# Performance work log

Measured on AMD Instinct MI355X. Metric: run time of the kernel, lower is better.

Reference implementation:

```python
import jax, jax.numpy as jnp
import numpy as np

SCORE_WEIGHT = 0.5
MAX_ITER = 20
PROJ_ITER = 5
RELAX_LR = 0.1
EPS = 1e-8

P, D, T, O, H, W = 256, 256, 2, 24, 240, 432


def setup_inputs() -> dict:
    key = jax.random.key(0)
    k1, k2, k3, k4, k5 = jax.random.split(key, 5)
    proposed_feature = jax.random.normal(k1, (P, D), dtype=jnp.float32)
    proposed_mask = (jax.random.uniform(k2, (P, H, W)) > 0.7).astype(jnp.float32)
    template_feature = jax.random.normal(k3, (T, O, D), dtype=jnp.float32)
    mask_last_occurence = (jax.random.uniform(k4, (O, H, W)) > 0.7).astype(jnp.float32)
    proposal_score = jax.random.uniform(k5, (P,), dtype=jnp.float32)
    return {
        "proposed_feature": proposed_feature,
        "proposed_mask": proposed_mask,
        "template_feature": template_feature,
        "mask_last_occurence": mask_last_occurence,
        "proposal_score": proposal_score,
    }


def relax_matching(C, max_iter=MAX_ITER, proj_iter=PROJ_INNER if False else PROJ_ITER, lr=RELAX_LR):
    """Projected-gradient relaxation of the assignment LP.
    Gradient step on <C, X>, then proj_iter alternating projections onto
    {X >= 0, X <= 1, row sums == 1}. Returns mean of iterates (sum(X_list)/len)."""
    K, N = C.shape
    X0 = jnp.full((K, N), 1.0 / N, dtype=C.dtype)

    def project(X):
        def body(_, X):
            X = jnp.clip(X, 0.0, 1.0)
            X = X / (jnp.sum(X, axis=1, keepdims=True) + EPS)
            return X
        return jax.lax.fori_loop(0, proj_iter, body, X)

    def step(X, _):
        X = project(X - lr * C)
        return X, X

    _, Xs = jax.lax.scan(step, X0, None, length=max_iter)
    return jnp.mean(Xs, axis=0)  # [K, N]


def reference(proposed_feature, proposed_mask, template_feature,
              mask_last_occurence, proposal_score):
    n_prop = proposed_mask.shape[0]
    n_tplt = mask_last_occurence.shape[0]
    h, w = proposed_mask.shape[1], proposed_mask.shape[2]

    # --- feature cosine similarity, averaged over template frames ---
    kf = proposed_feature / (jnp.linalg.norm(proposed_feature, axis=1, keepdims=True) + EPS)
    qf = template_feature / (jnp.linalg.norm(template_feature, axis=2, keepdims=True) + EPS)
    feature_sim = jnp.einsum('tod,pd->op', qf, kf) / template_feature.shape[0]  # [O, P]

    # --- pairwise binary-mask IoU without materializing [O*P, HW] ---
    A = mask_last_occurence.reshape(n_tplt, -1)  # [O, HW] templates
    B = proposed_mask.reshape(n_prop, -1)        # [P, HW] proposals
    inter = A @ B.T                              # [O, P]
    union = A.sum(axis=1)[:, None] + B.sum(axis=1)[None, :] - inter
    iou = inter / (union + EPS)

    sim_matrix = feature_sim * (1.0 - SCORE_WEIGHT) + iou * SCORE_WEIGHT
    # P > O so no padding branch; cost is [O, P]
    cost_matrix = -sim_matrix

    Ridx = relax_matching(cost_matrix)           # averaged iterates, [O, P]
    # training branch (is_test == 0)
    logic_mask = (Ridx > 0.01).astype(Ridx.dtype)
    binX = Ridx * logic_mask

    full_outmask = (binX @ B).reshape(n_tplt, h, w)                 # [O, H, W]
    match_score = jnp.max(jnp.clip(Ridx, 0.0, 1.0) * -cost_matrix, axis=1)  # [O]
    det_score = jnp.sum(proposal_score[None, :] * binX, axis=1)     # [O]
    return (full_outmask, match_score, det_score)
```

## Files before the change

### kernel.cpp

```cpp
#include <hip/hip_runtime.h>

#define HW 103680
#define WORDS 1620
#define NGRP 405
#define NP 256
#define NO 24
#define ND 256
#define EPSF 1e-8f
#define OUTM (NO*HW)

typedef unsigned long long u64;

__device__ __forceinline__ float waveRedSum(float v) {
  v += __int_as_float(__builtin_amdgcn_update_dpp(0, __float_as_int(v), 0x111, 0xf, 0xf, false));
  v += __int_as_float(__builtin_amdgcn_update_dpp(0, __float_as_int(v), 0x112, 0xf, 0xf, false));
  v += __int_as_float(__builtin_amdgcn_update_dpp(0, __float_as_int(v), 0x114, 0xf, 0xf, false));
  v += __int_as_float(__builtin_amdgcn_update_dpp(0, __float_as_int(v), 0x118, 0xf, 0xf, false));
  v += __int_as_float(__builtin_amdgcn_update_dpp(0, __float_as_int(v), 0x142, 0xf, 0xf, false));
  v += __int_as_float(__builtin_amdgcn_update_dpp(0, __float_as_int(v), 0x143, 0xf, 0xf, false));
  return __int_as_float(__builtin_amdgcn_readlane(__float_as_int(v), 63));
}
__device__ __forceinline__ float waveRedMax(float v) {
  int vi = __float_as_int(v);
  v = fmaxf(v, __int_as_float(__builtin_amdgcn_update_dpp(vi, vi, 0x111, 0xf, 0xf, false))); vi = __float_as_int(v);
  v = fmaxf(v, __int_as_float(__builtin_amdgcn_update_dpp(vi, vi, 0x112, 0xf, 0xf, false))); vi = __float_as_int(v);
  v = fmaxf(v, __int_as_float(__builtin_amdgcn_update_dpp(vi, vi, 0x114, 0xf, 0xf, false))); vi = __float_as_int(v);
  v = fmaxf(v, __int_as_float(__builtin_amdgcn_update_dpp(vi, vi, 0x118, 0xf, 0xf, false))); vi = __float_as_int(v);
  v = fmaxf(v, __int_as_float(__builtin_amdgcn_update_dpp(vi, vi, 0x142, 0xf, 0xf, false))); vi = __float_as_int(v);
  v = fmaxf(v, __int_as_float(__builtin_amdgcn_update_dpp(vi, vi, 0x143, 0xf, 0xf, false)));
  return __int_as_float(__builtin_amdgcn_readlane(__float_as_int(v), 63));
}

__device__ __forceinline__ void pack_group(const float* __restrict__ rp,
                                           u64* __restrict__ bits,
                                           int g, int lane, float4 v) {
  u64 m0 = __ballot(v.x != 0.0f);
  u64 m1 = __ballot(v.y != 0.0f);
  u64 m2 = __ballot(v.z != 0.0f);
  u64 m3 = __ballot(v.w != 0.0f);
  if (lane == 0) {
    ulonglong2 s0; s0.x = m0; s0.y = m1;
    ulonglong2 s1; s1.x = m2; s1.y = m3;
    *(ulonglong2*)(bits + g * 4)     = s0;
    *(ulonglong2*)(bits + g * 4 + 2) = s1;
  }
}

__global__ __launch_bounds__(256) void pack_kernel(const float* __restrict__ pm,
                                                   const float* __restrict__ ml,
                                                   u64* __restrict__ bbits,
                                                   u64* __restrict__ abits) {
  int row = blockIdx.y;
  int wir = (blockIdx.x * 256 + threadIdx.x) >> 6;
  int lane = threadIdx.x & 63;
  const float* rp;
  u64* bits;
  if (row < NP) { rp = pm + (size_t)row * HW;        bits = bbits + (size_t)row * WORDS; }
  else          { rp = ml + (size_t)(row - NP) * HW; bits = abits + (size_t)(row - NP) * WORDS; }
  int g = wir;
  while (g + 28 < NGRP) {
    float4 v0 = *(const float4*)(rp + g * 256 + lane * 4);
    float4 v1 = *(const float4*)(rp + (g + 28) * 256 + lane * 4);
    pack_group(rp, bits, g, lane, v0);
    pack_group(rp, bits, g + 28, lane, v1);
    g += 56;
  }
  if (g < NGRP) {
    float4 v0 = *(const float4*)(rp + g * 256 + lane * 4);
    pack_group(rp, bits, g, lane, v0);
  }
}

__global__ __launch_bounds__(256) void interfeat_kernel(const u64* __restrict__ ab,
                                                        const u64* __restrict__ bb,
                                                        const float* __restrict__ pf,
                                                        const float* __restrict__ tf,
                                                        float* __restrict__ C) {
  int wid = (blockIdx.x * 256 + threadIdx.x) >> 6;
  int lane = threadIdx.x & 63;
  int o = wid >> 8, p = wid & 255;
  float4 f = *(const float4*)(pf + p * ND + lane * 4);
  float4 a = *(const float4*)(tf + o * ND + lane * 4);
  float4 b = *(const float4*)(tf + (NO + o) * ND + lane * 4);
  const u64* arl = ab + (size_t)o * WORDS + lane;
  const u64* brl = bb + (size_t)p * WORDS + lane;
  int cnt = 0, ucnt = 0;
#pragma unroll 5
  for (int k = 0; k < 25; ++k) {
    u64 av = arl[k * 64], bv = brl[k * 64];
    cnt  += (int)__popcll(av & bv);
    ucnt += (int)__popcll(av | bv);
  }
  if (lane < WORDS - 1600) {
    u64 av = arl[1600], bv = brl[1600];
    cnt  += (int)__popcll(av & bv);
    ucnt += (int)__popcll(av | bv);
  }
  float inter = waveRedSum((float)cnt);
  float uni   = waveRedSum((float)ucnt);
  float nf = waveRedSum(f.x*f.x + f.y*f.y + f.z*f.z + f.w*f.w);
  float na = waveRedSum(a.x*a.x + a.y*a.y + a.z*a.z + a.w*a.w);
  float nb = waveRedSum(b.x*b.x + b.y*b.y + b.z*b.z + b.w*b.w);
  float d0 = waveRedSum(a.x*f.x + a.y*f.y + a.z*f.z + a.w*f.w);
  float d1 = waveRedSum(b.x*f.x + b.y*f.y + b.z*f.z + b.w*f.w);
  if (lane == 0) {
    float invf = 1.0f / (sqrtf(nf) + EPSF);
    float inva = 1.0f / (sqrtf(na) + EPSF);
    float invb = 1.0f / (sqrtf(nb) + EPSF);
    float fs  = (d0 * inva + d1 * invb) * invf * 0.5f;
    float iou = inter / (uni + EPSF);
    C[wid] = -(fs * 0.5f + iou * 0.5f);
  }
}

__global__ __launch_bounds__(64) void solve_kernel(const float* __restrict__ Cm,
                                                   const float* __restrict__ score,
                                                   int* __restrict__ nzidx,
                                                   float* __restrict__ nzval,
                                                   int* __restrict__ nzcnt,
                                                   float* __restrict__ out) {
  int o = blockIdx.x, lane = threadIdx.x;
  float4 c4 = *(const float4*)(Cm + o * NP + lane * 4);
  float C[4] = {c4.x, c4.y, c4.z, c4.w};
  float sim[4], X[4], Xs[4];
#pragma unroll
  for (int j = 0; j < 4; ++j) {
    sim[j] = -C[j];
    X[j] = 1.0f / 256.0f;
    Xs[j] = 0.0f;
  }
  for (int it = 0; it < 20; ++it) {
#pragma unroll
    for (int j = 0; j < 4; ++j) X[j] = X[j] - 0.1f * C[j];
    for (int k = 0; k < 5; ++k) {
#pragma unroll
      for (int j = 0; j < 4; ++j) X[j] = fminf(fmaxf(X[j], 0.0f), 1.0f);
      float s = waveRedSum((X[0] + X[1]) + (X[2] + X[3]));
#pragma unroll
      for (int j = 0; j < 4; ++j) X[j] = X[j] / (s + EPSF);
    }
#pragma unroll
    for (int j = 0; j < 4; ++j) Xs[j] += X[j];
  }
  float R[4], bx[4];
#pragma unroll
  for (int j = 0; j < 4; ++j) {
    R[j] = Xs[j] / 20.0f;
    bx[j] = (R[j] > 0.01f) ? R[j] : 0.0f;
  }
  unsigned long long lt = (1ull << lane) - 1ull;
  int base = 0;
#pragma unroll
  for (int j = 0; j < 4; ++j) {
    unsigned long long m = __ballot(bx[j] != 0.0f);
    if (bx[j] != 0.0f) {
      int pos = base + (int)__popcll(m & lt);
      nzidx[o * NP + pos] = lane * 4 + j;
      nzval[o * NP + pos] = bx[j];
    }
    base += (int)__popcll(m);
  }
  if (lane == 0) nzcnt[o] = base;
  float mv = -1e30f;
#pragma unroll
  for (int j = 0; j < 4; ++j)
    mv = fmaxf(mv, fminf(fmaxf(R[j], 0.0f), 1.0f) * sim[j]);
  mv = waveRedMax(mv);
  float4 sc4 = *(const float4*)(score + lane * 4);
  float dv = waveRedSum(((sc4.x * bx[0]) + (sc4.y * bx[1])) + ((sc4.z * bx[2]) + (sc4.w * bx[3])));
  if (lane == 0) { out[OUTM + o] = mv; out[OUTM + NO + o] = dv; }
}

__global__ __launch_bounds__(256) void outmask_kernel(const u64* __restrict__ bb,
                                                      const int* __restrict__ nzidx,
                                                      const float* __restrict__ nzval,
                                                      const int* __restrict__ nzcnt,
                                                      float* __restrict__ out) {
  int o = blockIdx.y;
  int g = blockIdx.x * 4 + (threadIdx.x >> 6);
  int lane = threadIdx.x & 63;
  if (g >= NGRP) return;
  int cnt = nzcnt[o];
  float ax = 0.0f, ay = 0.0f, az = 0.0f, aw = 0.0f;
  for (int i = 0; i < cnt; ++i) {
    int p   = nzidx[o * NP + i];
    float v = nzval[o * NP + i];
    const u64* wp = bb + (size_t)p * WORDS + g * 4;
    u64 m0 = wp[0], m1 = wp[1], m2 = wp[2], m3 = wp[3];
    ax += ((m0 >> lane) & 1ull) ? v : 0.0f;
    ay += ((m1 >> lane) & 1ull) ? v : 0.0f;
    az += ((m2 >> lane) & 1ull) ? v : 0.0f;
    aw += ((m3 >> lane) & 1ull) ? v : 0.0f;
  }
  *(float4*)(out + (size_t)o * HW + g * 256 + lane * 4) = make_float4(ax, ay, az, aw);
}

extern "C" void kernel_launch(void* const* d_in, const int* in_sizes, int n_in,
                              void* d_out, int out_size, void* d_ws, size_t ws_size,
                              hipStream_t stream) {
  const float* pf = (const float*)d_in[0];
  const float* pm = (const float*)d_in[1];
  const float* tf = (const float*)d_in[2];
  const float* ml = (const float*)d_in[3];
  const float* sc = (const float*)d_in[4];
  float* out = (float*)d_out;
  char* ws = (char*)d_ws;

  u64*   bbits = (u64*)(ws);
  u64*   abits = (u64*)(ws + 3317760);
  int*   nzidx = (int*)(ws + 3317760);
  float* nzval = (float*)(ws + 3317760 + 24576);
  int*   nzcnt = (int*)(ws + 3317760 + 49152);
  float* Cm    = (float*)(ws + 3631136);

  hipLaunchKernelGGL(pack_kernel,      dim3(7, 280),  dim3(256), 0, stream, pm, ml, bbits, abits);
  hipLaunchKernelGGL(interfeat_kernel, dim3(1536),    dim3(256), 0, stream, abits, bbits, pf, tf, Cm);
  hipLaunchKernelGGL(solve_kernel,     dim3(24),      dim3(64),  0, stream, Cm, sc,
                     nzidx, nzval, nzcnt, out);
  hipLaunchKernelGGL(outmask_kernel,   dim3(102, 24), dim3(256), 0, stream, bbits, nzidx, nzval, nzcnt, out);
}
```

Baseline: 55.97 us.

## Fuse pack, IoU/feature, solve and outmask stages into one cooperative kernel

Replaces the four separate kernel launches with one persistent cooperative kernel of 512 blocks that separates the stages with grid-wide barriers. Each wave walks a fixed strided share of the pack items, the cost-matrix entries and the outmask groups, so the inter-kernel launch gaps go away. The trade-off is that the bandwidth-heavy mask-packing phase now runs with a fixed, lower number of resident waves. The barriers add their own cost, and most of the grid idles while only 24 waves run the solver stage.

```diff
diff --git a/kernel.cpp b/kernel.cpp
--- a/kernel.cpp
+++ b/kernel.cpp
@@ -1,4 +1,7 @@
 #include <hip/hip_runtime.h>
+#include <hip/hip_cooperative_groups.h>
+
+namespace cg = cooperative_groups;
 
 #define HW 103680
 #define WORDS 1620
@@ -8,6 +11,11 @@
 #define ND 256
 #define EPSF 1e-8f
 #define OUTM (NO*HW)
+#define NBLK 512
+#define NWAVE (NBLK*4)
+#define PACK_ITEMS (280*NGRP)
+#define PACK_PER_WAVE 56
+#define OUT_ITEMS (NO*NGRP)
 
 typedef unsigned long long u64;
 
@@ -31,168 +39,156 @@
   return __int_as_float(__builtin_amdgcn_readlane(__float_as_int(v), 63));
 }
 
-__device__ __forceinline__ void pack_group(const float* __restrict__ rp,
-                                           u64* __restrict__ bits,
-                                           int g, int lane, float4 v) {
-  u64 m0 = __ballot(v.x != 0.0f);
-  u64 m1 = __ballot(v.y != 0.0f);
-  u64 m2 = __ballot(v.z != 0.0f);
-  u64 m3 = __ballot(v.w != 0.0f);
-  if (lane == 0) {
-    ulonglong2 s0; s0.x = m0; s0.y = m1;
-    ulonglong2 s1; s1.x = m2; s1.y = m3;
-    *(ulonglong2*)(bits + g * 4)     = s0;
-    *(ulonglong2*)(bits + g * 4 + 2) = s1;
-  }
-}
-
-__global__ __launch_bounds__(256) void pack_kernel(const float* __restrict__ pm,
-                                                   const float* __restrict__ ml,
-                                                   u64* __restrict__ bbits,
-                                                   u64* __restrict__ abits) {
-  int row = blockIdx.y;
-  int wir = (blockIdx.x * 256 + threadIdx.x) >> 6;
-  int lane = threadIdx.x & 63;
-  const float* rp;
-  u64* bits;
-  if (row < NP) { rp = pm + (size_t)row * HW;        bits = bbits + (size_t)row * WORDS; }
-  else          { rp = ml + (size_t)(row - NP) * HW; bits = abits + (size_t)(row - NP) * WORDS; }
-  int g = wir;
-  while (g + 28 < NGRP) {
-    float4 v0 = *(const float4*)(rp + g * 256 + lane * 4);
-    float4 v1 = *(const float4*)(rp + (g + 28) * 256 + lane * 4);
-    pack_group(rp, bits, g, lane, v0);
-    pack_group(rp, bits, g + 28, lane, v1);
-    g += 56;
-  }
-  if (g < NGRP) {
-    float4 v0 = *(const float4*)(rp + g * 256 + lane * 4);
-    pack_group(rp, bits, g, lane, v0);
-  }
-}
-
-__global__ __launch_bounds__(256) void interfeat_kernel(const u64* __restrict__ ab,
-                                                        const u64* __restrict__ bb,
-                                                        const float* __restrict__ pf,
-                                                        const float* __restrict__ tf,
-                                                        float* __restrict__ C) {
-  int wid = (blockIdx.x * 256 + threadIdx.x) >> 6;
-  int lane = threadIdx.x & 63;
-  int o = wid >> 8, p = wid & 255;
-  float4 f = *(const float4*)(pf + p * ND + lane * 4);
-  float4 a = *(const float4*)(tf + o * ND + lane * 4);
-  float4 b = *(const float4*)(tf + (NO + o) * ND + lane * 4);
-  const u64* arl = ab + (size_t)o * WORDS + lane;
-  const u64* brl = bb + (size_t)p * WORDS + lane;
-  int cnt = 0, ucnt = 0;
+__global__ __launch_bounds__(256, 4) void fused_kernel(
+    const float* __restrict__ pf, const float* __restrict__ pm,
+    const float* __restrict__ tf, const float* __restrict__ ml,
+    const float* __restrict__ sc, float* __restrict__ out,
+    u64* __restrict__ bbits, u64* __restrict__ abits,
+    int* __restrict__ nzidx, float* __restrict__ nzval,
+    int* __restrict__ nzcnt, float* __restrict__ Cm) {
+  cg::grid_group grid = cg::this_grid();
+  int tid = threadIdx.x;
+  int lane = tid & 63;
+  int W = blockIdx.x * 4 + (tid >> 6);
+
+  {
+    int i0 = W * PACK_PER_WAVE;
+#pragma unroll 2
+    for (int j = 0; j < PACK_PER_WAVE; ++j) {
+      int i = i0 + j;
+      if (i >= PACK_ITEMS) break;
+      int row = i / NGRP;
+      int g = i - row * NGRP;
+      const float* rp; u64* bits;
+      if (row < NP) { rp = pm + (size_t)row * HW;        bits = bbits + (size_t)row * WORDS; }
+      else          { rp = ml + (size_t)(row - NP) * HW; bits = abits + (size_t)(row - NP) * WORDS; }
+      float4 v = *(const float4*)(rp + g * 256 + lane * 4);
+      u64 m0 = __ballot(v.x != 0.0f);
+      u64 m1 = __ballot(v.y != 0.0f);
+      u64 m2 = __ballot(v.z != 0.0f);
+      u64 m3 = __ballot(v.w != 0.0f);
+      if (lane == 0) {
+        ulonglong2 s0; s0.x = m0; s0.y = m1;
+        ulonglong2 s1; s1.x = m2; s1.y = m3;
+        *(ulonglong2*)(bits + g * 4)     = s0;
+        *(ulonglong2*)(bits + g * 4 + 2) = s1;
+      }
+    }
+  }
+  grid.sync();
+
+  {
+#pragma unroll 1
+    for (int q = 0; q < 3; ++q) {
+      int wid = W + q * NWAVE;
+      int o = wid >> 8, p = wid & 255;
+      float4 f = *(const float4*)(pf + p * ND + lane * 4);
+      float4 a = *(const float4*)(tf + o * ND + lane * 4);
+      float4 b = *(const float4*)(tf + (NO + o) * ND + lane * 4);
+      const u64* arl = abits + (size_t)o * WORDS + lane;
+      const u64* brl = bbits + (size_t)p * WORDS + lane;
+      int cnt = 0, ucnt = 0;
 #pragma unroll 5
-  for (int k = 0; k < 25; ++k) {
-    u64 av = arl[k * 64], bv = brl[k * 64];
-    cnt  += (int)__popcll(av & bv);
-    ucnt += (int)__popcll(av | bv);
-  }
-  if (lane < WORDS - 1600) {
-    u64 av = arl[1600], bv = brl[1600];
-    cnt  += (int)__popcll(av & bv);
-    ucnt += (int)__popcll(av | bv);
-  }
-  float inter = waveRedSum((float)cnt);
-  float uni   = waveRedSum((float)ucnt);
-  float nf = waveRedSum(f.x*f.x + f.y*f.y + f.z*f.z + f.w*f.w);
-  float na = waveRedSum(a.x*a.x + a.y*a.y + a.z*a.z + a.w*a.w);
-  float nb = waveRedSum(b.x*b.x + b.y*b.y + b.z*b.z + b.w*b.w);
-  float d0 = waveRedSum(a.x*f.x + a.y*f.y + a.z*f.z + a.w*f.w);
-  float d1 = waveRedSum(b.x*f.x + b.y*f.y + b.z*f.z + b.w*f.w);
-  if (lane == 0) {
-    float invf = 1.0f / (sqrtf(nf) + EPSF);
-    float inva = 1.0f / (sqrtf(na) + EPSF);
-    float invb = 1.0f / (sqrtf(nb) + EPSF);
-    float fs  = (d0 * inva + d1 * invb) * invf * 0.5f;
-    float iou = inter / (uni + EPSF);
-    C[wid] = -(fs * 0.5f + iou * 0.5f);
-  }
-}
-
-__global__ __launch_bounds__(64) void solve_kernel(const float* __restrict__ Cm,
-                                                   const float* __restrict__ score,
-                                                   int* __restrict__ nzidx,
-                                                   float* __restrict__ nzval,
-                                                   int* __restrict__ nzcnt,
-                                                   float* __restrict__ out) {
-  int o = blockIdx.x, lane = threadIdx.x;
-  float4 c4 = *(const float4*)(Cm + o * NP + lane * 4);
-  float C[4] = {c4.x, c4.y, c4.z, c4.w};
-  float sim[4], X[4], Xs[4];
-#pragma unroll
-  for (int j = 0; j < 4; ++j) {
-    sim[j] = -C[j];
-    X[j] = 1.0f / 256.0f;
-    Xs[j] = 0.0f;
-  }
-  for (int it = 0; it < 20; ++it) {
-#pragma unroll
-    for (int j = 0; j < 4; ++j) X[j] = X[j] - 0.1f * C[j];
-    for (int k = 0; k < 5; ++k) {
-#pragma unroll
-      for (int j = 0; j < 4; ++j) X[j] = fminf(fmaxf(X[j], 0.0f), 1.0f);
-      float s = waveRedSum((X[0] + X[1]) + (X[2] + X[3]));
-#pragma unroll
-      for (int j = 0; j < 4; ++j) X[j] = X[j] / (s + EPSF);
-    }
-#pragma unroll
-    for (int j = 0; j < 4; ++j) Xs[j] += X[j];
-  }
-  float R[4], bx[4];
-#pragma unroll
-  for (int j = 0; j < 4; ++j) {
-    R[j] = Xs[j] / 20.0f;
-    bx[j] = (R[j] > 0.01f) ? R[j] : 0.0f;
-  }
-  unsigned long long lt = (1ull << lane) - 1ull;
-  int base = 0;
-#pragma unroll
-  for (int j = 0; j < 4; ++j) {
-    unsigned long long m = __ballot(bx[j] != 0.0f);
-    if (bx[j] != 0.0f) {
-      int pos = base + (int)__popcll(m & lt);
-      nzidx[o * NP + pos] = lane * 4 + j;
-      nzval[o * NP + pos] = bx[j];
-    }
-    base += (int)__popcll(m);
-  }
-  if (lane == 0) nzcnt[o] = base;
-  float mv = -1e30f;
-#pragma unroll
-  for (int j = 0; j < 4; ++j)
-    mv = fmaxf(mv, fminf(fmaxf(R[j], 0.0f), 1.0f) * sim[j]);
-  mv = waveRedMax(mv);
-  float4 sc4 = *(const float4*)(score + lane * 4);
-  float dv = waveRedSum(((sc4.x * bx[0]) + (sc4.y * bx[1])) + ((sc4.z * bx[2]) + (sc4.w * bx[3])));
-  if (lane == 0) { out[OUTM + o] = mv; out[OUTM + NO + o] = dv; }
-}
-
-__global__ __launch_bounds__(256) void outmask_kernel(const u64* __restrict__ bb,
-                                                      const int* __restrict__ nzidx,
-                                                      const float* __restrict__ nzval,
-                                                      const int* __restrict__ nzcnt,
-                                                      float* __restrict__ out) {
-  int o = blockIdx.y;
-  int g = blockIdx.x * 4 + (threadIdx.x >> 6);
-  int lane = threadIdx.x & 63;
-  if (g >= NGRP) return;
-  int cnt = nzcnt[o];
-  float ax = 0.0f, ay = 0.0f, az = 0.0f, aw = 0.0f;
-  for (int i = 0; i < cnt; ++i) {
-    int p   = nzidx[o * NP + i];
-    float v = nzval[o * NP + i];
-    const u64* wp = bb + (size_t)p * WORDS + g * 4;
-    u64 m0 = wp[0], m1 = wp[1], m2 = wp[2], m3 = wp[3];
-    ax += ((m0 >> lane) & 1ull) ? v : 0.0f;
-    ay += ((m1 >> lane) & 1ull) ? v : 0.0f;
-    az += ((m2 >> lane) & 1ull) ? v : 0.0f;
-    aw += ((m3 >> lane) & 1ull) ? v : 0.0f;
-  }
-  *(float4*)(out + (size_t)o * HW + g * 256 + lane * 4) = make_float4(ax, ay, az, aw);
+      for (int k = 0; k < 25; ++k) {
+        u64 av = arl[k * 64], bv = brl[k * 64];
+        cnt  += (int)__popcll(av & bv);
+        ucnt += (int)__popcll(av | bv);
+      }
+      if (lane < WORDS - 1600) {
+        u64 av = arl[1600], bv = brl[1600];
+        cnt  += (int)__popcll(av & bv);
+        ucnt += (int)__popcll(av | bv);
+      }
+      float inter = waveRedSum((float)cnt);
+      float uni   = waveRedSum((float)ucnt);
+      float nf = waveRedSum(f.x*f.x + f.y*f.y + f.z*f.z + f.w*f.w);
+      float na = waveRedSum(a.x*a.x + a.y*a.y + a.z*a.z + a.w*a.w);
+      float nb = waveRedSum(b.x*b.x + b.y*b.y + b.z*b.z + b.w*b.w);
+      float d0 = waveRedSum(a.x*f.x + a.y*f.y + a.z*f.z + a.w*f.w);
+      float d1 = waveRedSum(b.x*f.x + b.y*f.y + b.z*f.z + b.w*f.w);
+      if (lane == 0) {
+        float invf = 1.0f / (sqrtf(nf) + EPSF);
+        float inva = 1.0f / (sqrtf(na) + EPSF);
+        float invb = 1.0f / (sqrtf(nb) + EPSF);
+        float fs  = (d0 * inva + d1 * invb) * invf * 0.5f;
+        float iou = inter / (uni + EPSF);
+        Cm[wid] = -(fs * 0.5f + iou * 0.5f);
+      }
+    }
+  }
+  grid.sync();
+
+  if (W < NO) {
+    int o = W;
+    float4 c4 = *(const float4*)(Cm + o * NP + lane * 4);
+    float C[4] = {c4.x, c4.y, c4.z, c4.w};
+    float sim[4], X[4], Xs[4];
+#pragma unroll
+    for (int j = 0; j < 4; ++j) {
+      sim[j] = -C[j];
+      X[j] = 1.0f / 256.0f;
+      Xs[j] = 0.0f;
+    }
+    for (int it = 0; it < 20; ++it) {
+#pragma unroll
+      for (int j = 0; j < 4; ++j) X[j] = X[j] - 0.1f * C[j];
+      for (int k = 0; k < 5; ++k) {
+#pragma unroll
+        for (int j = 0; j < 4; ++j) X[j] = fminf(fmaxf(X[j], 0.0f), 1.0f);
+        float s = waveRedSum((X[0] + X[1]) + (X[2] + X[3]));
+#pragma unroll
+        for (int j = 0; j < 4; ++j) X[j] = X[j] / (s + EPSF);
+      }
+#pragma unroll
+      for (int j = 0; j < 4; ++j) Xs[j] += X[j];
+    }
+    float R[4], bx[4];
+#pragma unroll
+    for (int j = 0; j < 4; ++j) {
+      R[j] = Xs[j] / 20.0f;
+      bx[j] = (R[j] > 0.01f) ? R[j] : 0.0f;
+    }
+    unsigned long long lt = (1ull << lane) - 1ull;
+    int base = 0;
+#pragma unroll
+    for (int j = 0; j < 4; ++j) {
+      unsigned long long m = __ballot(bx[j] != 0.0f);
+      if (bx[j] != 0.0f) {
+        int pos = base + (int)__popcll(m & lt);
+        nzidx[o * NP + pos] = lane * 4 + j;
+        nzval[o * NP + pos] = bx[j];
+      }
+      base += (int)__popcll(m);
+    }
+    if (lane == 0) nzcnt[o] = base;
+    float mv = -1e30f;
+#pragma unroll
+    for (int j = 0; j < 4; ++j)
+      mv = fmaxf(mv, fminf(fmaxf(R[j], 0.0f), 1.0f) * sim[j]);
+    mv = waveRedMax(mv);
+    float4 sc4 = *(const float4*)(sc + lane * 4);
+    float dv = waveRedSum(((sc4.x * bx[0]) + (sc4.y * bx[1])) + ((sc4.z * bx[2]) + (sc4.w * bx[3])));
+    if (lane == 0) { out[OUTM + o] = mv; out[OUTM + NO + o] = dv; }
+  }
+  grid.sync();
+
+  for (int i = W; i < OUT_ITEMS; i += NWAVE) {
+    int o = i / NGRP;
+    int g = i - o * NGRP;
+    int cnt = nzcnt[o];
+    float ax = 0.0f, ay = 0.0f, az = 0.0f, aw = 0.0f;
+    for (int t = 0; t < cnt; ++t) {
+      int p   = nzidx[o * NP + t];
+      float v = nzval[o * NP + t];
+      const u64* wp = bbits + (size_t)p * WORDS + g * 4;
+      u64 m0 = wp[0], m1 = wp[1], m2 = wp[2], m3 = wp[3];
+      ax += ((m0 >> lane) & 1ull) ? v : 0.0f;
+      ay += ((m1 >> lane) & 1ull) ? v : 0.0f;
+      az += ((m2 >> lane) & 1ull) ? v : 0.0f;
+      aw += ((m3 >> lane) & 1ull) ? v : 0.0f;
+    }
+    *(float4*)(out + (size_t)o * HW + g * 256 + lane * 4) = make_float4(ax, ay, az, aw);
+  }
 }
 
 extern "C" void kernel_launch(void* const* d_in, const int* in_sizes, int n_in,
@@ -213,9 +209,9 @@
   int*   nzcnt = (int*)(ws + 3317760 + 49152);
   float* Cm    = (float*)(ws + 3631136);
 
-  hipLaunchKernelGGL(pack_kernel,      dim3(7, 280),  dim3(256), 0, stream, pm, ml, bbits, abits);
-  hipLaunchKernelGGL(interfeat_kernel, dim3(1536),    dim3(256), 0, stream, abits, bbits, pf, tf, Cm);
-  hipLaunchKernelGGL(solve_kernel,     dim3(24),      dim3(64),  0, stream, Cm, sc,
-                     nzidx, nzval, nzcnt, out);
-  hipLaunchKernelGGL(outmask_kernel,   dim3(102, 24), dim3(256), 0, stream, bbits, nzidx, nzval, nzcnt, out);
-}
+  void* args[] = {(void*)&pf, (void*)&pm, (void*)&tf, (void*)&ml, (void*)&sc,
+                  (void*)&out, (void*)&bbits, (void*)&abits,
+                  (void*)&nzidx, (void*)&nzval, (void*)&nzcnt, (void*)&Cm};
+  hipLaunchCooperativeKernel((const void*)fused_kernel, dim3(NBLK), dim3(256),
+                             args, 0, stream);
+}
```

Result: slower. 211.0 us (+277.0%).

## Fuse solver with outmask kernel and restructure mask bit-packing with nontemporal loads

Applied to the files above, without the earlier changes.

Merges the assignment solver and the output-mask expansion into one kernel of 24 blocks with 1024 threads. Wave 0 solves and writes the nonzero list to shared memory, then all 16 waves expand the masks. This removes a launch and a global round trip for the nonzero list. The pack kernel now gives each wave a 16-group chunk, uses nontemporal loads, and writes one coalesced 64-bit word per lane instead of lane-0 stores. The risk is that the outmask phase now runs on only 24 blocks instead of 2448, which greatly reduces parallelism for writing the roughly 10 MB output.

```diff
diff --git a/kernel.cpp b/kernel.cpp
--- a/kernel.cpp
+++ b/kernel.cpp
@@ -8,8 +8,10 @@
 #define ND 256
 #define EPSF 1e-8f
 #define OUTM (NO*HW)
+#define NCHUNK 26
 
 typedef unsigned long long u64;
+typedef float vfloat4 __attribute__((ext_vector_type(4)));
 
 __device__ __forceinline__ float waveRedSum(float v) {
   v += __int_as_float(__builtin_amdgcn_update_dpp(0, __float_as_int(v), 0x111, 0xf, 0xf, false));
@@ -31,43 +33,44 @@
   return __int_as_float(__builtin_amdgcn_readlane(__float_as_int(v), 63));
 }
 
-__device__ __forceinline__ void pack_group(const float* __restrict__ rp,
-                                           u64* __restrict__ bits,
-                                           int g, int lane, float4 v) {
-  u64 m0 = __ballot(v.x != 0.0f);
-  u64 m1 = __ballot(v.y != 0.0f);
-  u64 m2 = __ballot(v.z != 0.0f);
-  u64 m3 = __ballot(v.w != 0.0f);
-  if (lane == 0) {
-    ulonglong2 s0; s0.x = m0; s0.y = m1;
-    ulonglong2 s1; s1.x = m2; s1.y = m3;
-    *(ulonglong2*)(bits + g * 4)     = s0;
-    *(ulonglong2*)(bits + g * 4 + 2) = s1;
-  }
-}
-
 __global__ __launch_bounds__(256) void pack_kernel(const float* __restrict__ pm,
                                                    const float* __restrict__ ml,
                                                    u64* __restrict__ bbits,
                                                    u64* __restrict__ abits) {
-  int row = blockIdx.y;
-  int wir = (blockIdx.x * 256 + threadIdx.x) >> 6;
+  int W = blockIdx.x * 4 + (threadIdx.x >> 6);
   int lane = threadIdx.x & 63;
-  const float* rp;
-  u64* bits;
+  int row = W / NCHUNK;
+  int cidx = W - row * NCHUNK;
+  const float* rp; u64* bits;
   if (row < NP) { rp = pm + (size_t)row * HW;        bits = bbits + (size_t)row * WORDS; }
   else          { rp = ml + (size_t)(row - NP) * HW; bits = abits + (size_t)(row - NP) * WORDS; }
-  int g = wir;
-  while (g + 28 < NGRP) {
-    float4 v0 = *(const float4*)(rp + g * 256 + lane * 4);
-    float4 v1 = *(const float4*)(rp + (g + 28) * 256 + lane * 4);
-    pack_group(rp, bits, g, lane, v0);
-    pack_group(rp, bits, g + 28, lane, v1);
-    g += 56;
-  }
-  if (g < NGRP) {
-    float4 v0 = *(const float4*)(rp + g * 256 + lane * 4);
-    pack_group(rp, bits, g, lane, v0);
+  int g0 = cidx * 16;
+  int k4 = lane >> 2, c = lane & 3;
+  u64 myword = 0;
+  if (cidx != 25) {
+#pragma unroll
+    for (int k = 0; k < 16; ++k) {
+      vfloat4 v = __builtin_nontemporal_load((const vfloat4*)(rp + (size_t)(g0 + k) * 256 + lane * 4));
+      u64 m0 = __ballot(v.x != 0.0f);
+      u64 m1 = __ballot(v.y != 0.0f);
+      u64 m2 = __ballot(v.z != 0.0f);
+      u64 m3 = __ballot(v.w != 0.0f);
+      u64 s = (c == 0) ? m0 : (c == 1) ? m1 : (c == 2) ? m2 : m3;
+      if (k4 == k) myword = s;
+    }
+    bits[g0 * 4 + lane] = myword;
+  } else {
+#pragma unroll
+    for (int k = 0; k < 5; ++k) {
+      vfloat4 v = __builtin_nontemporal_load((const vfloat4*)(rp + (size_t)(g0 + k) * 256 + lane * 4));
+      u64 m0 = __ballot(v.x != 0.0f);
+      u64 m1 = __ballot(v.y != 0.0f);
+      u64 m2 = __ballot(v.z != 0.0f);
+      u64 m3 = __ballot(v.w != 0.0f);
+      u64 s = (c == 0) ? m0 : (c == 1) ? m1 : (c == 2) ? m2 : m3;
+      if (k4 == k) myword = s;
+    }
+    if (lane < 20) bits[g0 * 4 + lane] = myword;
   }
 }
 
@@ -113,86 +116,84 @@
   }
 }
 
-__global__ __launch_bounds__(64) void solve_kernel(const float* __restrict__ Cm,
-                                                   const float* __restrict__ score,
-                                                   int* __restrict__ nzidx,
-                                                   float* __restrict__ nzval,
-                                                   int* __restrict__ nzcnt,
-                                                   float* __restrict__ out) {
-  int o = blockIdx.x, lane = threadIdx.x;
-  float4 c4 = *(const float4*)(Cm + o * NP + lane * 4);
-  float C[4] = {c4.x, c4.y, c4.z, c4.w};
-  float sim[4], X[4], Xs[4];
-#pragma unroll
-  for (int j = 0; j < 4; ++j) {
-    sim[j] = -C[j];
-    X[j] = 1.0f / 256.0f;
-    Xs[j] = 0.0f;
-  }
-  for (int it = 0; it < 20; ++it) {
-#pragma unroll
-    for (int j = 0; j < 4; ++j) X[j] = X[j] - 0.1f * C[j];
-    for (int k = 0; k < 5; ++k) {
-#pragma unroll
-      for (int j = 0; j < 4; ++j) X[j] = fminf(fmaxf(X[j], 0.0f), 1.0f);
-      float s = waveRedSum((X[0] + X[1]) + (X[2] + X[3]));
-#pragma unroll
-      for (int j = 0; j < 4; ++j) X[j] = X[j] / (s + EPSF);
-    }
-#pragma unroll
-    for (int j = 0; j < 4; ++j) Xs[j] += X[j];
-  }
-  float R[4], bx[4];
-#pragma unroll
-  for (int j = 0; j < 4; ++j) {
-    R[j] = Xs[j] / 20.0f;
-    bx[j] = (R[j] > 0.01f) ? R[j] : 0.0f;
-  }
-  unsigned long long lt = (1ull << lane) - 1ull;
-  int base = 0;
-#pragma unroll
-  for (int j = 0; j < 4; ++j) {
-    unsigned long long m = __ballot(bx[j] != 0.0f);
-    if (bx[j] != 0.0f) {
-      int pos = base + (int)__popcll(m & lt);
-      nzidx[o * NP + pos] = lane * 4 + j;
-      nzval[o * NP + pos] = bx[j];
-    }
-    base += (int)__popcll(m);
-  }
-  if (lane == 0) nzcnt[o] = base;
-  float mv = -1e30f;
-#pragma unroll
-  for (int j = 0; j < 4; ++j)
-    mv = fmaxf(mv, fminf(fmaxf(R[j], 0.0f), 1.0f) * sim[j]);
-  mv = waveRedMax(mv);
-  float4 sc4 = *(const float4*)(score + lane * 4);
-  float dv = waveRedSum(((sc4.x * bx[0]) + (sc4.y * bx[1])) + ((sc4.z * bx[2]) + (sc4.w * bx[3])));
-  if (lane == 0) { out[OUTM + o] = mv; out[OUTM + NO + o] = dv; }
-}
-
-__global__ __launch_bounds__(256) void outmask_kernel(const u64* __restrict__ bb,
-                                                      const int* __restrict__ nzidx,
-                                                      const float* __restrict__ nzval,
-                                                      const int* __restrict__ nzcnt,
-                                                      float* __restrict__ out) {
-  int o = blockIdx.y;
-  int g = blockIdx.x * 4 + (threadIdx.x >> 6);
-  int lane = threadIdx.x & 63;
-  if (g >= NGRP) return;
-  int cnt = nzcnt[o];
-  float ax = 0.0f, ay = 0.0f, az = 0.0f, aw = 0.0f;
-  for (int i = 0; i < cnt; ++i) {
-    int p   = nzidx[o * NP + i];
-    float v = nzval[o * NP + i];
-    const u64* wp = bb + (size_t)p * WORDS + g * 4;
-    u64 m0 = wp[0], m1 = wp[1], m2 = wp[2], m3 = wp[3];
-    ax += ((m0 >> lane) & 1ull) ? v : 0.0f;
-    ay += ((m1 >> lane) & 1ull) ? v : 0.0f;
-    az += ((m2 >> lane) & 1ull) ? v : 0.0f;
-    aw += ((m3 >> lane) & 1ull) ? v : 0.0f;
-  }
-  *(float4*)(out + (size_t)o * HW + g * 256 + lane * 4) = make_float4(ax, ay, az, aw);
+__global__ __launch_bounds__(1024) void solmask_kernel(const float* __restrict__ Cm,
+                                                       const float* __restrict__ score,
+                                                       const u64* __restrict__ bb,
+                                                       float* __restrict__ out) {
+  int o = blockIdx.x;
+  int tid = threadIdx.x, lane = tid & 63, w = tid >> 6;
+  __shared__ int   s_nzidx[NP];
+  __shared__ float s_nzval[NP];
+  __shared__ int   s_nzcnt;
+
+  if (w == 0) {
+    float4 c4 = *(const float4*)(Cm + o * NP + lane * 4);
+    float C[4] = {c4.x, c4.y, c4.z, c4.w};
+    float sim[4], X[4], Xs[4];
+#pragma unroll
+    for (int j = 0; j < 4; ++j) {
+      sim[j] = -C[j];
+      X[j] = 1.0f / 256.0f;
+      Xs[j] = 0.0f;
+    }
+    for (int it = 0; it < 20; ++it) {
+#pragma unroll
+      for (int j = 0; j < 4; ++j) X[j] = X[j] - 0.1f * C[j];
+      for (int k = 0; k < 5; ++k) {
+#pragma unroll
+        for (int j = 0; j < 4; ++j) X[j] = fminf(fmaxf(X[j], 0.0f), 1.0f);
+        float s = waveRedSum((X[0] + X[1]) + (X[2] + X[3]));
+#pragma unroll
+        for (int j = 0; j < 4; ++j) X[j] = X[j] / (s + EPSF);
+      }
+#pragma unroll
+      for (int j = 0; j < 4; ++j) Xs[j] += X[j];
+    }
+    float R[4], bx[4];
+#pragma unroll
+    for (int j = 0; j < 4; ++j) {
+      R[j] = Xs[j] / 20.0f;
+      bx[j] = (R[j] > 0.01f) ? R[j] : 0.0f;
+    }
+    unsigned long long lt = (1ull << lane) - 1ull;
+    int base = 0;
+#pragma unroll
+    for (int j = 0; j < 4; ++j) {
+      unsigned long long m = __ballot(bx[j] != 0.0f);
+      if (bx[j] != 0.0f) {
+        int pos = base + (int)__popcll(m & lt);
+        s_nzidx[pos] = lane * 4 + j;
+        s_nzval[pos] = bx[j];
+      }
+      base += (int)__popcll(m);
+    }
+    if (lane == 0) s_nzcnt = base;
+    float mv = -1e30f;
+#pragma unroll
+    for (int j = 0; j < 4; ++j)
+      mv = fmaxf(mv, fminf(fmaxf(R[j], 0.0f), 1.0f) * sim[j]);
+    mv = waveRedMax(mv);
+    float4 sc4 = *(const float4*)(score + lane * 4);
+    float dv = waveRedSum(((sc4.x * bx[0]) + (sc4.y * bx[1])) + ((sc4.z * bx[2]) + (sc4.w * bx[3])));
+    if (lane == 0) { out[OUTM + o] = mv; out[OUTM + NO + o] = dv; }
+  }
+  __syncthreads();
+
+  int cnt = s_nzcnt;
+  for (int g = w; g < NGRP; g += 16) {
+    float ax = 0.0f, ay = 0.0f, az = 0.0f, aw = 0.0f;
+    for (int t = 0; t < cnt; ++t) {
+      int p   = s_nzidx[t];
+      float v = s_nzval[t];
+      const u64* wp = bb + (size_t)p * WORDS + g * 4;
+      u64 m0 = wp[0], m1 = wp[1], m2 = wp[2], m3 = wp[3];
+      ax += ((m0 >> lane) & 1ull) ? v : 0.0f;
+      ay += ((m1 >> lane) & 1ull) ? v : 0.0f;
+      az += ((m2 >> lane) & 1ull) ? v : 0.0f;
+      aw += ((m3 >> lane) & 1ull) ? v : 0.0f;
+    }
+    *(float4*)(out + (size_t)o * HW + g * 256 + lane * 4) = make_float4(ax, ay, az, aw);
+  }
 }
 
 extern "C" void kernel_launch(void* const* d_in, const int* in_sizes, int n_in,
@@ -208,14 +209,9 @@
 
   u64*   bbits = (u64*)(ws);
   u64*   abits = (u64*)(ws + 3317760);
-  int*   nzidx = (int*)(ws + 3317760);
-  float* nzval = (float*)(ws + 3317760 + 24576);
-  int*   nzcnt = (int*)(ws + 3317760 + 49152);
-  float* Cm    = (float*)(ws + 3631136);
-
-  hipLaunchKernelGGL(pack_kernel,      dim3(7, 280),  dim3(256), 0, stream, pm, ml, bbits, abits);
-  hipLaunchKernelGGL(interfeat_kernel, dim3(1536),    dim3(256), 0, stream, abits, bbits, pf, tf, Cm);
-  hipLaunchKernelGGL(solve_kernel,     dim3(24),      dim3(64),  0, stream, Cm, sc,
-                     nzidx, nzval, nzcnt, out);
-  hipLaunchKernelGGL(outmask_kernel,   dim3(102, 24), dim3(256), 0, stream, bbits, nzidx, nzval, nzcnt, out);
-}
+  float* Cm    = (float*)(ws + 3628800);
+
+  hipLaunchKernelGGL(pack_kernel,      dim3(1820), dim3(256),  0, stream, pm, ml, bbits, abits);
+  hipLaunchKernelGGL(interfeat_kernel, dim3(1536), dim3(256),  0, stream, abits, bbits, pf, tf, Cm);
+  hipLaunchKernelGGL(solmask_kernel,   dim3(24),   dim3(1024), 0, stream, Cm, sc, bbits, out);
+}
```

New measurement: 54.64 us. 2.4% less time.
